# Optimization experiments

Hardware: AMD Instinct MI355X
Metric: run time of the kernel (lower is better)

## Reference

```python
import jax, jax.numpy as jnp
import numpy as np

EPS = 0.1          # entropic regularization (init eps)
MAX_ITER = 20      # Sinkhorn iterations (init max_iter)
THRESH = 0.1       # convergence threshold on err (from torch source)
COS_EPS = 1e-8     # CosineSimilarity eps


def setup_inputs() -> dict:
    key = jax.random.key(0)
    kx, ky = jax.random.split(key)
    B, N, M, D = 4, 1024, 1024, 512
    x = jax.random.normal(kx, (B, N, D), dtype=jnp.float32)
    y = jax.random.normal(ky, (B, M, D), dtype=jnp.float32)
    nu = jnp.full((B, M), 1.0 / M, dtype=jnp.float32)  # target marginal
    return {"x": x, "y": y, "nu": nu}


def _cost_matrix(x, y):
    # C_ij = 1 - cos(x_i, y_j), with torch CosineSimilarity eps semantics
    dot = jnp.einsum("bnd,bmd->bnm", x, y)
    nx = jnp.linalg.norm(x, axis=-1)  # [B, N]
    ny = jnp.linalg.norm(y, axis=-1)  # [B, M]
    denom = jnp.maximum(nx[:, :, None] * ny[:, None, :], COS_EPS)
    return 1.0 - dot / denom  # [B, N, M]


def reference(x, y, nu):
    C = _cost_matrix(x, y)  # [B, N, M]
    B, N, _ = C.shape
    log_mu = jnp.log(jnp.full((B, N), 1.0 / N, dtype=C.dtype) + 1e-8)  # [B, N]
    log_nu = jnp.log(nu + 1e-8)  # [B, M]

    def Mmat(u, v):
        # M_ij = (-C_ij + u_i + v_j) / eps
        return (-C + u[:, :, None] + v[:, None, :]) / EPS

    def step(carry, _):
        u, v, done = carry
        u_new = EPS * (log_mu - jax.scipy.special.logsumexp(Mmat(u, v), axis=-1)) + u
        v_new = EPS * (log_nu - jax.scipy.special.logsumexp(Mmat(u_new, v), axis=-2)) + v
        err = jnp.abs(u_new - u).sum(-1).mean()
        # freeze updates after convergence (emulates the host-side break)
        u2 = jnp.where(done, u, u_new)
        v2 = jnp.where(done, v, v_new)
        return (u2, v2, done | (err < THRESH)), None

    u0 = jnp.zeros_like(log_mu)
    v0 = jnp.zeros_like(log_nu)
    (u, v, _), _ = jax.lax.scan(step, (u0, v0, jnp.array(False)), None, length=MAX_ITER)

    pi = jnp.exp(Mmat(u, v))  # transport plan [B, N, M]
    cost = jnp.sum(pi * C, axis=(-2, -1))  # [B]  (reduction='none')
    return cost
```

## Files before the change

kernel.cpp:

```cpp
#include <hip/hip_runtime.h>
#include <math.h>

#define EPS      0.1f
#define INV_EPS  10.0f
#define THRESH   0.1f
#define MAX_IT   20

#define BB 4
#define NN 1024
#define MM 1024
#define DD 512

#define MU_P (1.0f / 1024.0f + 1e-8f)

#define GBLK 128
#define TBLK 512

#define OFF_K    ((size_t)0)
#define OFF_XB   ((size_t)2097152)
#define OFF_YB   ((size_t)3145728)
#define OFF_NX   ((size_t)4194304)
#define OFF_NY   (OFF_NX + 4096)
#define OFF_NUP  (OFF_NY + 4096)
#define OFF_CS   (OFF_NUP + 4096)
#define OFF_FLG  (OFF_CS + 12288)

#define GLDA 40

typedef __bf16 bf16x8 __attribute__((ext_vector_type(8)));
typedef float f32x4 __attribute__((ext_vector_type(4)));
typedef unsigned long long u64;

__device__ __forceinline__ float wave_reduce_sum(float x) {
#pragma unroll
  for (int off = 32; off > 0; off >>= 1) x += __shfl_xor(x, off, 64);
  return x;
}

__device__ __forceinline__ uint pk2(float a, float b) {
  __bf16 ha = (__bf16)a, hb = (__bf16)b;
  return (uint)*(ushort*)&ha | ((uint)*(ushort*)&hb << 16);
}

__global__ void __launch_bounds__(256) prep_kernel(const float* __restrict__ x,
                                                   const float* __restrict__ y,
                                                   ushort* __restrict__ xb,
                                                   ushort* __restrict__ yb,
                                                   float* __restrict__ nx,
                                                   float* __restrict__ ny,
                                                   const float* __restrict__ nu,
                                                   float* nup, float* colsum,
                                                   int* flagsi, float* out) {
  const int tid = threadIdx.x;
  int gt = blockIdx.x * 256 + tid;
  if (gt < BB * MM) {
    nup[gt] = nu[gt] + 1e-8f;
    colsum[4096 + gt] = 0.f;
  }
  if (gt < 512) flagsi[gt] = 0;
  if (gt < BB) out[gt] = 0.f;

  const int w = tid >> 6, lane = tid & 63;
  const int r = blockIdx.x * 4 + w;
  const bool isx = (r < BB * NN);
  const float* src = isx ? (x + (size_t)r * DD)
                         : (y + (size_t)(r - BB * NN) * DD);
  ushort* dst = isx ? (xb + (size_t)r * DD)
                    : (yb + (size_t)(r - BB * NN) * DD);
  const float4* s4 = (const float4*)src;
  float4 a = s4[lane * 2];
  float4 b = s4[lane * 2 + 1];
  float ss = a.x * a.x + a.y * a.y + a.z * a.z + a.w * a.w +
             b.x * b.x + b.y * b.y + b.z * b.z + b.w * b.w;
  uint4 pk = make_uint4(pk2(a.x, a.y), pk2(a.z, a.w), pk2(b.x, b.y), pk2(b.z, b.w));
  *(uint4*)(dst + lane * 8) = pk;
  ss = wave_reduce_sum(ss);
  if (lane == 0) {
    float n = sqrtf(ss);
    if (isx) nx[r] = n; else ny[r - BB * NN] = n;
  }
}

__global__ void __launch_bounds__(256) gemm_kernel(const ushort* __restrict__ xb,
                                                   const ushort* __restrict__ yb,
                                                   const float* __restrict__ nxg,
                                                   const float* __restrict__ nyg,
                                                   ushort* __restrict__ K) {
  __shared__ ushort Ah[128 * GLDA];
  __shared__ ushort Bh[128 * GLDA];
  __shared__ float s_nx[128], s_ny[128];

  const int b = blockIdx.z;
  const int i0 = blockIdx.y * 128;
  const int j0 = blockIdx.x * 128;
  const int t = threadIdx.x;
  const int w = t >> 6, lane = t & 63;
  const int m16 = lane & 15, q = lane >> 4;
  const int wm = (w & 1) * 64, wn = (w >> 1) * 64;

  const int srow = t >> 1;
  const int soff = (t & 1) * 16;

  const ushort* xrow = xb + ((size_t)b * NN + i0 + srow) * DD + soff;
  const ushort* yrow = yb + ((size_t)b * MM + j0 + srow) * DD + soff;

  f32x4 acc[4][4];
#pragma unroll
  for (int mi = 0; mi < 4; ++mi)
#pragma unroll
    for (int ni = 0; ni < 4; ++ni) acc[mi][ni] = (f32x4)0.f;

  for (int k0 = 0; k0 < DD; k0 += 32) {
    uint4 av0 = *(const uint4*)(xrow + k0);
    uint4 av1 = *(const uint4*)(xrow + k0 + 8);
    uint4 bv0 = *(const uint4*)(yrow + k0);
    uint4 bv1 = *(const uint4*)(yrow + k0 + 8);
    __syncthreads();
    *(uint4*)&Ah[srow * GLDA + soff] = av0;
    *(uint4*)&Ah[srow * GLDA + soff + 8] = av1;
    *(uint4*)&Bh[srow * GLDA + soff] = bv0;
    *(uint4*)&Bh[srow * GLDA + soff + 8] = bv1;
    __syncthreads();

    bf16x8 ahf[4], bhf[4];
#pragma unroll
    for (int mi = 0; mi < 4; ++mi)
      ahf[mi] = *(const bf16x8*)&Ah[(wm + mi * 16 + m16) * GLDA + q * 8];
#pragma unroll
    for (int ni = 0; ni < 4; ++ni)
      bhf[ni] = *(const bf16x8*)&Bh[(wn + ni * 16 + m16) * GLDA + q * 8];
#pragma unroll
    for (int mi = 0; mi < 4; ++mi)
#pragma unroll
      for (int ni = 0; ni < 4; ++ni)
        acc[mi][ni] = __builtin_amdgcn_mfma_f32_16x16x32_bf16(ahf[mi], bhf[ni], acc[mi][ni], 0, 0, 0);
  }

  if (t < 128) s_nx[t] = nxg[b * NN + i0 + t];
  else s_ny[t - 128] = nyg[b * MM + j0 + t - 128];
  __syncthreads();

#pragma unroll
  for (int mi = 0; mi < 4; ++mi)
#pragma unroll
    for (int ni = 0; ni < 4; ++ni)
#pragma unroll
      for (int r = 0; r < 4; ++r) {
        const int m = wm + mi * 16 + q * 4 + r;
        const int n = wn + ni * 16 + m16;
        float den = fmaxf(s_nx[m] * s_ny[n], 1e-8f);
        float cv = 1.0f - acc[mi][ni][r] / den;
        float kf = __expf(-cv * INV_EPS);
        __bf16 hb = (__bf16)kf;
        K[((size_t)b * NN + i0 + m) * MM + j0 + n] = *(ushort*)&hb;
      }
}

__device__ __forceinline__ void unpack8(uint4 k, float* kf) {
  kf[0] = __uint_as_float(k.x << 16);
  kf[1] = __uint_as_float(k.x & 0xffff0000u);
  kf[2] = __uint_as_float(k.y << 16);
  kf[3] = __uint_as_float(k.y & 0xffff0000u);
  kf[4] = __uint_as_float(k.z << 16);
  kf[5] = __uint_as_float(k.z & 0xffff0000u);
  kf[6] = __uint_as_float(k.w << 16);
  kf[7] = __uint_as_float(k.w & 0xffff0000u);
}

__global__ void __launch_bounds__(TBLK) sinkhorn_kernel(
    const ushort* __restrict__ K, float* __restrict__ colsum,
    const float* __restrict__ nup, u64* __restrict__ flags,
    float* __restrict__ out) {
  const int tid = threadIdx.x;
  const int bid = blockIdx.x;
  const int lane = tid & 63;
  const int w = tid >> 6;
  const int b = bid >> 5;
  const int rbase = (bid & 31) * 32;

  __shared__ float swv[1024];
  __shared__ float spart[8][1024];
  __shared__ float s_red;
  __shared__ int s_conv;

  const float eps_log_mu = EPS * __logf(MU_P);
  float u_prev[4] = {0.f, 0.f, 0.f, 0.f};
  float wu_reg[4] = {0.f, 0.f, 0.f, 0.f};
  int T = 0;

  for (int it = 0; it < MAX_IT; ++it) {
    const int genv = it + 1;
    if (tid == 0) s_red = 0.f;
    if (it == 0) {
      swv[tid] = 1.f;
      swv[tid + 512] = 1.f;
    } else {
      const float* cs = colsum + (it % 3) * 4096 + b * MM;
      float c0 = __hip_atomic_load(cs + tid, __ATOMIC_RELAXED, __HIP_MEMORY_SCOPE_AGENT);
      float c1 = __hip_atomic_load(cs + tid + 512, __ATOMIC_RELAXED, __HIP_MEMORY_SCOPE_AGENT);
      swv[tid] = nup[b * MM + tid] / c0;
      swv[tid + 512] = nup[b * MM + tid + 512] / c1;
    }
    __syncthreads();

    float wvr[16];
    {
      const float4* wp = (const float4*)swv;
      *(float4*)&wvr[0] = wp[lane * 2];
      *(float4*)&wvr[4] = wp[lane * 2 + 1];
      *(float4*)&wvr[8] = wp[128 + lane * 2];
      *(float4*)&wvr[12] = wp[129 + lane * 2];
    }
    float creg[16];
#pragma unroll
    for (int t2 = 0; t2 < 16; ++t2) creg[t2] = 0.f;

    uint4 kq[4][2];
#pragma unroll
    for (int rr = 0; rr < 4; ++rr) {
      const uint4* kp = (const uint4*)(K + ((size_t)b * NN + rbase + w * 4 + rr) * MM);
      kq[rr][0] = kp[lane];
      kq[rr][1] = kp[lane + 64];
    }

    float werr = 0.f;
#pragma unroll
    for (int rr = 0; rr < 4; ++rr) {
      float kf[16];
      unpack8(kq[rr][0], kf);
      unpack8(kq[rr][1], kf + 8);
      float s = 0.f;
#pragma unroll
      for (int t2 = 0; t2 < 16; ++t2) s = fmaf(kf[t2], wvr[t2], s);
      s = wave_reduce_sum(s);
      float unv = eps_log_mu - EPS * __logf(s);
      werr += fabsf(unv - u_prev[rr]);
      u_prev[rr] = unv;
      float wu = MU_P / s;
      wu_reg[rr] = wu;
#pragma unroll
      for (int t2 = 0; t2 < 16; ++t2) creg[t2] = fmaf(wu, kf[t2], creg[t2]);
    }
    if (lane == 0) atomicAdd(&s_red, werr);

    {
      float* pr = &spart[w][0];
      *(float4*)&pr[lane * 8] = *(float4*)&creg[0];
      *(float4*)&pr[lane * 8 + 4] = *(float4*)&creg[4];
      *(float4*)&pr[512 + lane * 8] = *(float4*)&creg[8];
      *(float4*)&pr[512 + lane * 8 + 4] = *(float4*)&creg[12];
    }
    __syncthreads();

    {
      float* csn = colsum + ((it + 1) % 3) * 4096 + b * MM;
      const int j0 = tid * 2;
      float s0 = 0.f, s1 = 0.f;
#pragma unroll
      for (int ww = 0; ww < 8; ++ww) {
        float2 p = *(const float2*)&spart[ww][j0];
        s0 += p.x;
        s1 += p.y;
      }
      unsafeAtomicAdd(&csn[j0], s0);
      unsafeAtomicAdd(&csn[j0 + 1], s1);
      if (tid < 32) {
        float* csz = colsum + ((it + 2) % 3) * 4096;
        __hip_atomic_store(&csz[bid * 32 + tid], 0.f, __ATOMIC_RELAXED, __HIP_MEMORY_SCOPE_AGENT);
      }
    }

    asm volatile("s_waitcnt vmcnt(0)" ::: "memory");
    __syncthreads();
    if (tid == 0) {
      u64 f = ((u64)(uint)genv << 32) | (u64)__float_as_uint(s_red);
      __hip_atomic_store(&flags[(genv & 1) * GBLK + bid], f, __ATOMIC_RELAXED, __HIP_MEMORY_SCOPE_AGENT);
    }
    if (tid < 64) {
      const u64* fl = flags + (genv & 1) * GBLK;
      u64 f0, f1;
      for (;;) {
        f0 = __hip_atomic_load(fl + tid, __ATOMIC_RELAXED, __HIP_MEMORY_SCOPE_AGENT);
        f1 = __hip_atomic_load(fl + tid + 64, __ATOMIC_RELAXED, __HIP_MEMORY_SCOPE_AGENT);
        if (__all(((f0 >> 32) >= (u64)genv) && ((f1 >> 32) >= (u64)genv))) break;
        __builtin_amdgcn_s_sleep(1);
      }
      float e = __uint_as_float((uint)f0) + __uint_as_float((uint)f1);
      e = wave_reduce_sum(e);
      if (tid == 0) s_conv = (e * (1.0f / (float)BB) < THRESH) ? 1 : 0;
    }
    __syncthreads();
    T = it;
    if (s_conv) break;
  }

  {
    const float* cs = colsum + ((T + 1) % 3) * 4096 + b * MM;
    float c0 = __hip_atomic_load(cs + tid, __ATOMIC_RELAXED, __HIP_MEMORY_SCOPE_AGENT);
    float c1 = __hip_atomic_load(cs + tid + 512, __ATOMIC_RELAXED, __HIP_MEMORY_SCOPE_AGENT);
    swv[tid] = nup[b * MM + tid] / c0;
    swv[tid + 512] = nup[b * MM + tid + 512] / c1;
  }
  if (tid == 0) s_red = 0.f;
  __syncthreads();

  float wvr[16];
  {
    const float4* wp = (const float4*)swv;
    *(float4*)&wvr[0] = wp[lane * 2];
    *(float4*)&wvr[4] = wp[lane * 2 + 1];
    *(float4*)&wvr[8] = wp[128 + lane * 2];
    *(float4*)&wvr[12] = wp[129 + lane * 2];
  }

  float wcost = 0.f;
#pragma unroll
  for (int rr = 0; rr < 4; ++rr) {
    const int r = rbase + w * 4 + rr;
    const uint4* kp = (const uint4*)(K + ((size_t)b * NN + r) * MM);
    uint4 k0 = kp[lane], k1 = kp[lane + 64];
    float kf[16];
    unpack8(k0, kf);
    unpack8(k1, kf + 8);
    float s = 0.f;
#pragma unroll
    for (int t2 = 0; t2 < 16; ++t2)
      s = fmaf(kf[t2] * wvr[t2], -EPS * __logf(kf[t2]), s);
    s = wave_reduce_sum(s) * wu_reg[rr];
    if (lane == 0) wcost += s;
  }
  if (lane == 0) atomicAdd(&s_red, wcost);
  __syncthreads();
  if (tid == 0) atomicAdd(out + b, s_red);
}

extern "C" void kernel_launch(void* const* d_in, const int* in_sizes, int n_in,
                              void* d_out, int out_size, void* d_ws, size_t ws_size,
                              hipStream_t stream) {
  const float* x = (const float*)d_in[0];
  const float* y = (const float*)d_in[1];
  const float* nu = (const float*)d_in[2];
  float* out = (float*)d_out;
  float* ws = (float*)d_ws;

  ushort* K = (ushort*)(ws + OFF_K);
  ushort* xb = (ushort*)(ws + OFF_XB);
  ushort* yb = (ushort*)(ws + OFF_YB);
  float* nx = ws + OFF_NX;
  float* ny = ws + OFF_NY;
  float* nup = ws + OFF_NUP;
  float* cs = ws + OFF_CS;
  u64* flg = (u64*)(ws + OFF_FLG);

  prep_kernel<<<2048, 256, 0, stream>>>(x, y, xb, yb, nx, ny, nu, nup, cs, (int*)flg, out);
  gemm_kernel<<<dim3(8, 8, 4), 256, 0, stream>>>(xb, yb, nx, ny, K);

  void* args[] = {(void*)&K, (void*)&cs, (void*)&nup, (void*)&flg, (void*)&out};
  hipLaunchCooperativeKernel(reinterpret_cast<void*>(&sinkhorn_kernel),
                             dim3(GBLK), dim3(TBLK), args, 0, stream);
}
```

Baseline: 126.9 us.

## Replace grid-wide barrier with per-batch barrier and defer convergence check

```diff
diff --git a/kernel.cpp b/kernel.cpp
--- a/kernel.cpp
+++ b/kernel.cpp
@@ -22,8 +22,9 @@
 #define OFF_NX   ((size_t)4194304)
 #define OFF_NY   (OFF_NX + 4096)
 #define OFF_NUP  (OFF_NY + 4096)
-#define OFF_CS   (OFF_NUP + 4096)
-#define OFF_FLG  (OFF_CS + 12288)
+#define OFF_ERRB (OFF_NUP + 4096)
+#define OFF_CS   (OFF_ERRB + 2560)
+#define OFF_FLG  (OFF_CS + 81920)
 
 #define GLDA 40
 
@@ -49,14 +50,12 @@
                                                    float* __restrict__ nx,
                                                    float* __restrict__ ny,
                                                    const float* __restrict__ nu,
-                                                   float* nup, float* colsum,
+                                                   float* nup, float* cs_all,
                                                    int* flagsi, float* out) {
   const int tid = threadIdx.x;
   int gt = blockIdx.x * 256 + tid;
-  if (gt < BB * MM) {
-    nup[gt] = nu[gt] + 1e-8f;
-    colsum[4096 + gt] = 0.f;
-  }
+  if (gt < BB * MM) nup[gt] = nu[gt] + 1e-8f;
+  if (gt < MAX_IT * BB * MM) cs_all[gt] = 0.f;
   if (gt < 512) flagsi[gt] = 0;
   if (gt < BB) out[gt] = 0.f;
 
@@ -167,10 +166,14 @@
   kf[7] = __uint_as_float(k.w & 0xffff0000u);
 }
 
+__device__ __forceinline__ float agl(const float* p) {
+  return __hip_atomic_load(p, __ATOMIC_RELAXED, __HIP_MEMORY_SCOPE_AGENT);
+}
+
 __global__ void __launch_bounds__(TBLK) sinkhorn_kernel(
-    const ushort* __restrict__ K, float* __restrict__ colsum,
-    const float* __restrict__ nup, u64* __restrict__ flags,
-    float* __restrict__ out) {
+    const ushort* __restrict__ K, float* __restrict__ CS,
+    const float* __restrict__ nup, float* __restrict__ errbuf,
+    u64* __restrict__ flags, float* __restrict__ out) {
   const int tid = threadIdx.x;
   const int bid = blockIdx.x;
   const int lane = tid & 63;
@@ -178,51 +181,52 @@
   const int b = bid >> 5;
   const int rbase = (bid & 31) * 32;
 
-  __shared__ float swv[1024];
   __shared__ float spart[8][1024];
+  __shared__ float sErr[MAX_IT];
   __shared__ float s_red;
-  __shared__ int s_conv;
 
   const float eps_log_mu = EPS * __logf(MU_P);
+
+  uint4 kq[4][2];
+#pragma unroll
+  for (int rr = 0; rr < 4; ++rr) {
+    const uint4* kp = (const uint4*)(K + ((size_t)b * NN + rbase + w * 4 + rr) * MM);
+    kq[rr][0] = kp[lane];
+    kq[rr][1] = kp[lane + 64];
+  }
+  float nupr[16];
+  {
+    const float4* np4 = (const float4*)(nup + b * MM);
+    *(float4*)&nupr[0] = np4[lane * 2];
+    *(float4*)&nupr[4] = np4[lane * 2 + 1];
+    *(float4*)&nupr[8] = np4[128 + lane * 2];
+    *(float4*)&nupr[12] = np4[129 + lane * 2];
+  }
+
   float u_prev[4] = {0.f, 0.f, 0.f, 0.f};
-  float wu_reg[4] = {0.f, 0.f, 0.f, 0.f};
-  int T = 0;
+  float wvr[16];
+
+  if (tid == 0) s_red = 0.f;
+  __syncthreads();
 
   for (int it = 0; it < MAX_IT; ++it) {
     const int genv = it + 1;
-    if (tid == 0) s_red = 0.f;
     if (it == 0) {
-      swv[tid] = 1.f;
-      swv[tid + 512] = 1.f;
+#pragma unroll
+      for (int t2 = 0; t2 < 16; ++t2) wvr[t2] = 1.f;
     } else {
-      const float* cs = colsum + (it % 3) * 4096 + b * MM;
-      float c0 = __hip_atomic_load(cs + tid, __ATOMIC_RELAXED, __HIP_MEMORY_SCOPE_AGENT);
-      float c1 = __hip_atomic_load(cs + tid + 512, __ATOMIC_RELAXED, __HIP_MEMORY_SCOPE_AGENT);
-      swv[tid] = nup[b * MM + tid] / c0;
-      swv[tid + 512] = nup[b * MM + tid + 512] / c1;
-    }
-    __syncthreads();
-
-    float wvr[16];
-    {
-      const float4* wp = (const float4*)swv;
-      *(float4*)&wvr[0] = wp[lane * 2];
-      *(float4*)&wvr[4] = wp[lane * 2 + 1];
-      *(float4*)&wvr[8] = wp[128 + lane * 2];
-      *(float4*)&wvr[12] = wp[129 + lane * 2];
-    }
+      const float* cs = CS + ((size_t)(it - 1) * BB + b) * MM;
+#pragma unroll
+      for (int t2 = 0; t2 < 8; ++t2)
+        wvr[t2] = nupr[t2] * __builtin_amdgcn_rcpf(agl(cs + lane * 8 + t2));
+#pragma unroll
+      for (int t2 = 0; t2 < 8; ++t2)
+        wvr[8 + t2] = nupr[8 + t2] * __builtin_amdgcn_rcpf(agl(cs + 512 + lane * 8 + t2));
+    }
+
     float creg[16];
 #pragma unroll
     for (int t2 = 0; t2 < 16; ++t2) creg[t2] = 0.f;
-
-    uint4 kq[4][2];
-#pragma unroll
-    for (int rr = 0; rr < 4; ++rr) {
-      const uint4* kp = (const uint4*)(K + ((size_t)b * NN + rbase + w * 4 + rr) * MM);
-      kq[rr][0] = kp[lane];
-      kq[rr][1] = kp[lane + 64];
-    }
-
     float werr = 0.f;
 #pragma unroll
     for (int rr = 0; rr < 4; ++rr) {
@@ -237,7 +241,6 @@
       werr += fabsf(unv - u_prev[rr]);
       u_prev[rr] = unv;
       float wu = MU_P / s;
-      wu_reg[rr] = wu;
 #pragma unroll
       for (int t2 = 0; t2 < 16; ++t2) creg[t2] = fmaf(wu, kf[t2], creg[t2]);
     }
@@ -253,7 +256,7 @@
     __syncthreads();
 
     {
-      float* csn = colsum + ((it + 1) % 3) * 4096 + b * MM;
+      float* csn = CS + ((size_t)it * BB + b) * MM;
       const int j0 = tid * 2;
       float s0 = 0.f, s1 = 0.f;
 #pragma unroll
@@ -264,69 +267,97 @@
       }
       unsafeAtomicAdd(&csn[j0], s0);
       unsafeAtomicAdd(&csn[j0 + 1], s1);
-      if (tid < 32) {
-        float* csz = colsum + ((it + 2) % 3) * 4096;
-        __hip_atomic_store(&csz[bid * 32 + tid], 0.f, __ATOMIC_RELAXED, __HIP_MEMORY_SCOPE_AGENT);
+    }
+    if (tid == 0)
+      __hip_atomic_store(errbuf + it * GBLK + bid, s_red, __ATOMIC_RELAXED, __HIP_MEMORY_SCOPE_AGENT);
+
+    asm volatile("s_waitcnt vmcnt(0)" ::: "memory");
+    __syncthreads();
+    if (tid == 0) {
+      u64 f = ((u64)(uint)genv << 32);
+      __hip_atomic_store(&flags[(genv & 1) * GBLK + bid], f, __ATOMIC_RELAXED, __HIP_MEMORY_SCOPE_AGENT);
+      s_red = 0.f;
+    }
+    if (tid < 64) {
+      const u64* fl = flags + (genv & 1) * GBLK + b * 32;
+      for (;;) {
+        u64 f0 = __hip_atomic_load(fl + (tid & 31), __ATOMIC_RELAXED, __HIP_MEMORY_SCOPE_AGENT);
+        if (__all((f0 >> 32) >= (u64)genv)) break;
+        __builtin_amdgcn_s_sleep(1);
       }
     }
-
-    asm volatile("s_waitcnt vmcnt(0)" ::: "memory");
-    __syncthreads();
+    __syncthreads();
+  }
+
+  {
+    const int genv = MAX_IT + 1;
     if (tid == 0) {
-      u64 f = ((u64)(uint)genv << 32) | (u64)__float_as_uint(s_red);
+      u64 f = ((u64)(uint)genv << 32);
       __hip_atomic_store(&flags[(genv & 1) * GBLK + bid], f, __ATOMIC_RELAXED, __HIP_MEMORY_SCOPE_AGENT);
     }
     if (tid < 64) {
       const u64* fl = flags + (genv & 1) * GBLK;
-      u64 f0, f1;
       for (;;) {
-        f0 = __hip_atomic_load(fl + tid, __ATOMIC_RELAXED, __HIP_MEMORY_SCOPE_AGENT);
-        f1 = __hip_atomic_load(fl + tid + 64, __ATOMIC_RELAXED, __HIP_MEMORY_SCOPE_AGENT);
+        u64 f0 = __hip_atomic_load(fl + tid, __ATOMIC_RELAXED, __HIP_MEMORY_SCOPE_AGENT);
+        u64 f1 = __hip_atomic_load(fl + tid + 64, __ATOMIC_RELAXED, __HIP_MEMORY_SCOPE_AGENT);
         if (__all(((f0 >> 32) >= (u64)genv) && ((f1 >> 32) >= (u64)genv))) break;
         __builtin_amdgcn_s_sleep(1);
       }
-      float e = __uint_as_float((uint)f0) + __uint_as_float((uint)f1);
+    }
+    __syncthreads();
+  }
+
+  if (tid < 64) {
+    for (int t = 0; t < MAX_IT; ++t) {
+      float e = agl(errbuf + t * GBLK + tid) + agl(errbuf + t * GBLK + 64 + tid);
       e = wave_reduce_sum(e);
-      if (tid == 0) s_conv = (e * (1.0f / (float)BB) < THRESH) ? 1 : 0;
-    }
-    __syncthreads();
-    T = it;
-    if (s_conv) break;
-  }
-
+      if (tid == 0) sErr[t] = e;
+    }
+    if (tid == 0) s_red = 0.f;
+  }
+  __syncthreads();
+  int Tstar = MAX_IT - 1;
+  for (int t = 0; t < MAX_IT; ++t)
+    if (sErr[t] * (1.0f / (float)BB) < THRESH) { Tstar = t; break; }
+
+  float wvm1[16];
+  if (Tstar == 0) {
+#pragma unroll
+    for (int t2 = 0; t2 < 16; ++t2) wvm1[t2] = 1.f;
+  } else {
+    const float* cs = CS + ((size_t)(Tstar - 1) * BB + b) * MM;
+#pragma unroll
+    for (int t2 = 0; t2 < 8; ++t2)
+      wvm1[t2] = nupr[t2] * __builtin_amdgcn_rcpf(agl(cs + lane * 8 + t2));
+#pragma unroll
+    for (int t2 = 0; t2 < 8; ++t2)
+      wvm1[8 + t2] = nupr[8 + t2] * __builtin_amdgcn_rcpf(agl(cs + 512 + lane * 8 + t2));
+  }
   {
-    const float* cs = colsum + ((T + 1) % 3) * 4096 + b * MM;
-    float c0 = __hip_atomic_load(cs + tid, __ATOMIC_RELAXED, __HIP_MEMORY_SCOPE_AGENT);
-    float c1 = __hip_atomic_load(cs + tid + 512, __ATOMIC_RELAXED, __HIP_MEMORY_SCOPE_AGENT);
-    swv[tid] = nup[b * MM + tid] / c0;
-    swv[tid + 512] = nup[b * MM + tid + 512] / c1;
-  }
-  if (tid == 0) s_red = 0.f;
-  __syncthreads();
-
-  float wvr[16];
-  {
-    const float4* wp = (const float4*)swv;
-    *(float4*)&wvr[0] = wp[lane * 2];
-    *(float4*)&wvr[4] = wp[lane * 2 + 1];
-    *(float4*)&wvr[8] = wp[128 + lane * 2];
-    *(float4*)&wvr[12] = wp[129 + lane * 2];
+    const float* cs = CS + ((size_t)Tstar * BB + b) * MM;
+#pragma unroll
+    for (int t2 = 0; t2 < 8; ++t2)
+      wvr[t2] = nupr[t2] * __builtin_amdgcn_rcpf(agl(cs + lane * 8 + t2));
+#pragma unroll
+    for (int t2 = 0; t2 < 8; ++t2)
+      wvr[8 + t2] = nupr[8 + t2] * __builtin_amdgcn_rcpf(agl(cs + 512 + lane * 8 + t2));
   }
 
   float wcost = 0.f;
 #pragma unroll
   for (int rr = 0; rr < 4; ++rr) {
-    const int r = rbase + w * 4 + rr;
-    const uint4* kp = (const uint4*)(K + ((size_t)b * NN + r) * MM);
-    uint4 k0 = kp[lane], k1 = kp[lane + 64];
     float kf[16];
-    unpack8(k0, kf);
-    unpack8(k1, kf + 8);
-    float s = 0.f;
+    unpack8(kq[rr][0], kf);
+    unpack8(kq[rr][1], kf + 8);
+    float srow = 0.f, s = 0.f;
+#pragma unroll
+    for (int t2 = 0; t2 < 16; ++t2) srow = fmaf(kf[t2], wvm1[t2], srow);
+    srow = wave_reduce_sum(srow);
+    float wu = MU_P / srow;
 #pragma unroll
     for (int t2 = 0; t2 < 16; ++t2)
       s = fmaf(kf[t2] * wvr[t2], -EPS * __logf(kf[t2]), s);
-    s = wave_reduce_sum(s) * wu_reg[rr];
+    s = wave_reduce_sum(s) * wu;
     if (lane == 0) wcost += s;
   }
   if (lane == 0) atomicAdd(&s_red, wcost);
@@ -349,13 +380,14 @@
   float* nx = ws + OFF_NX;
   float* ny = ws + OFF_NY;
   float* nup = ws + OFF_NUP;
+  float* errb = ws + OFF_ERRB;
   float* cs = ws + OFF_CS;
   u64* flg = (u64*)(ws + OFF_FLG);
 
   prep_kernel<<<2048, 256, 0, stream>>>(x, y, xb, yb, nx, ny, nu, nup, cs, (int*)flg, out);
   gemm_kernel<<<dim3(8, 8, 4), 256, 0, stream>>>(xb, yb, nx, ny, K);
 
-  void* args[] = {(void*)&K, (void*)&cs, (void*)&nup, (void*)&flg, (void*)&out};
+  void* args[] = {(void*)&K, (void*)&cs, (void*)&nup, (void*)&errb, (void*)&flg, (void*)&out};
   hipLaunchCooperativeKernel(reinterpret_cast<void*>(&sinkhorn_kernel),
                              dim3(GBLK), dim3(TBLK), args, 0, stream);
 }
```

New measurement: 282.4 us. +122.6%, slower.
